# Kernel optimization log

Hardware: AMD Instinct MI355X
Metric: run time of the kernel (lower is better)

The kernel has to match this reference:

```python
import jax, jax.numpy as jnp
import numpy as np

C = 5.0          # tanh clamp constant (args.c, non-trainable)
B, N, R, D = 4, 16, 64, 256  # batch, block_num, block_len, word_dim
NEG = -1e9


def setup_inputs() -> dict:
    key = jax.random.key(0)
    ks = iter(jax.random.split(key, 80))

    def W(i, o):
        # xavier-like init (torch stores (out,in); we store (in,out) and use x @ W)
        return jax.random.normal(next(ks), (i, o), jnp.float32) * np.float32(np.sqrt(2.0 / (i + o)))

    def bvec(d):
        return jax.random.normal(next(ks), (d,), jnp.float32) * 0.01

    inp = {"x": jax.random.normal(next(ks), (B, N, R, D), jnp.float32)}
    for p in ("fw", "bw"):
        inp[f"fcW_{p}"] = W(D, D);  inp[f"fcb_{p}"] = bvec(D)
        inp[f"mW1_{p}"] = W(D, D);  inp[f"mW2_{p}"] = W(D, D);  inp[f"mb_{p}"] = bvec(D)
        inp[f"s2tW1_{p}"] = W(D, D); inp[f"s2tb1_{p}"] = bvec(D)
        inp[f"s2tW_{p}"] = W(D, D);  inp[f"s2tb_{p}"] = bvec(D)
        inp[f"gW1_{p}"] = W(D, D);  inp[f"gW2_{p}"] = W(D, D);  inp[f"gb_{p}"] = bvec(D)
        inp[f"fW1_{p}"] = W(3 * D, D); inp[f"fb1_{p}"] = bvec(D)
        inp[f"fW2_{p}"] = W(3 * D, D); inp[f"fb2_{p}"] = bvec(D)
    return inp


def _mSA(x, W1, W2, b, fw):
    # x: (..., L, d) -> (..., L, d). Additive per-feature attention with strict
    # triangular mask. fw: token i attends to j > i (last row zeroed);
    # bw: token i attends to j < i (first row zeroed). Matches the torch
    # -inf mask + narrow + zero-pad construction exactly.
    L = x.shape[-2]
    xi = (x @ W1)[..., :, None, :]                 # (..., L, 1, d)
    xj = (x @ W2)[..., None, :, :]                 # (..., 1, L, d)
    f = C * jnp.tanh((xi + xj + b) / C)            # (..., i, j, d)
    i = jnp.arange(L)[:, None]
    j = jnp.arange(L)[None, :]
    allowed = (j > i) if fw else (j < i)           # (L, L)
    scores = jnp.where(allowed[..., None], f, NEG)
    att = jax.nn.softmax(scores, axis=-2)          # softmax over j
    rowvalid = (jnp.arange(L) < L - 1) if fw else (jnp.arange(L) > 0)
    att = att * rowvalid[:, None, None].astype(x.dtype)
    return jnp.einsum('...ijd,...jd->...id', att, x)


def _s2t(x, W1, b1, Wo, bo):
    # source2token self-attention: (..., L, d) -> (..., d)
    f = jax.nn.relu(x @ W1 + b1)
    a = jax.nn.softmax(f @ Wo + bo, axis=-2)
    return jnp.sum(a * x, axis=-2)


def _mblosa(x, mW1, mW2, mb, s2tW1, s2tb1, s2tW, s2tb,
            gW1, gW2, gb, fW1, fb1, fW2, fb2, fw):
    Bb, n, r, d = x.shape
    h = _mSA(x, mW1, mW2, mb, fw)                  # (B, n, r, d) intra-block
    v = _s2t(h, s2tW1, s2tb1, s2tW, s2tb)          # (B, n, d)    block summary
    o = _mSA(v, mW1, mW2, mb, fw)                  # (B, n, d)    inter-block
    G = jax.nn.sigmoid(o @ gW1 + v @ gW2 + gb)
    e = G * o + (1.0 - G) * v                      # (B, n, d)
    # torch: cat of e[i] repeated r times, then narrow(1, 0, n)
    idx = jnp.arange(n) // r
    E = e[:, idx]                                  # (B, n, d)
    # torch: flatten blocks then narrow(1, 0, n) (faithful to source)
    xf = x.reshape(Bb, n * r, d)[:, :n]
    hf = h.reshape(Bb, n * r, d)[:, :n]
    cat = jnp.concatenate([xf, hf, E], axis=-1)    # (B, n, 3d)
    fusion = jax.nn.relu(cat @ fW1 + fb1)
    Gf = jax.nn.sigmoid(cat @ fW2 + fb2)
    return Gf * fusion + (1.0 - Gf) * xf           # (B, n, d)


def reference(x,
              fcW_fw, fcb_fw, mW1_fw, mW2_fw, mb_fw, s2tW1_fw, s2tb1_fw,
              s2tW_fw, s2tb_fw, gW1_fw, gW2_fw, gb_fw, fW1_fw, fb1_fw,
              fW2_fw, fb2_fw,
              fcW_bw, fcb_bw, mW1_bw, mW2_bw, mb_bw, s2tW1_bw, s2tb1_bw,
              s2tW_bw, s2tb_bw, gW1_bw, gW2_bw, gb_bw, fW1_bw, fb1_bw,
              fW2_bw, fb2_bw):
    in_fw = jax.nn.relu(x @ fcW_fw + fcb_fw)
    in_bw = jax.nn.relu(x @ fcW_bw + fcb_bw)
    u_fw = _mblosa(in_fw, mW1_fw, mW2_fw, mb_fw, s2tW1_fw, s2tb1_fw,
                   s2tW_fw, s2tb_fw, gW1_fw, gW2_fw, gb_fw,
                   fW1_fw, fb1_fw, fW2_fw, fb2_fw, True)
    u_bw = _mblosa(in_bw, mW1_bw, mW2_bw, mb_bw, s2tW1_bw, s2tb1_bw,
                   s2tW_bw, s2tb_bw, gW1_bw, gW2_bw, gb_bw,
                   fW1_bw, fb1_bw, fW2_bw, fb2_bw, False)
    return jnp.concatenate([u_fw, u_bw], axis=-1)  # (B, n, 2d)
```

## Files before the change

### kernel.cpp

```cpp
#include <hip/hip_runtime.h>
#include <hip/hip_bf16.h>

typedef __hip_bfloat16 BF16;
typedef __attribute__((ext_vector_type(8))) short short8;
typedef __attribute__((ext_vector_type(4))) float f32x4;

#define MFMA_B16(a,b,c) __builtin_amdgcn_mfma_f32_16x16x32_bf16((a),(b),(c),0,0,0)

#if __has_builtin(__builtin_amdgcn_exp2f)
#define EXP2F(x) __builtin_amdgcn_exp2f(x)
#else
#define EXP2F(x) __expf(0.6931471805599453f * (x))
#endif

__device__ __forceinline__ short f2bs(float f){ BF16 h = __float2bfloat16(f); return *(short*)&h; }
__device__ __forceinline__ float bs2f(short s){ BF16 h = *(BF16*)&s; return __bfloat162float(h); }

struct SrcPack { const float* s[10]; };

__global__ __launch_bounds__(256) void prep_k(SrcPack p, short* __restrict__ Oh,
                                              short* __restrict__ Ol)
{
    __shared__ float s[64][65];
    const float* W = p.s[blockIdx.y];
    short* oh = Oh + (size_t)blockIdx.y * 65536;
    short* ol = Ol + (size_t)blockIdx.y * 65536;
    int tr = (blockIdx.x >> 2) * 64, tc = (blockIdx.x & 3) * 64;
    #pragma unroll
    for (int i = 0; i < 16; i++) {
        int e = threadIdx.x + i * 256;
        int r = e >> 6, c = e & 63;
        s[c][r] = W[(size_t)(tr + r) * 256 + tc + c];
    }
    __syncthreads();
    #pragma unroll
    for (int i = 0; i < 16; i++) {
        int e = threadIdx.x + i * 256;
        int c2 = e >> 6, r2 = e & 63;
        float v = s[c2][r2];
        short hi = f2bs(v);
        short lo = f2bs(v - bs2f(hi));
        size_t oi = (size_t)(tc + c2) * 256 + tr + r2;
        oh[oi] = hi;
        ol[oi] = lo;
    }
}

template<int AM, int OM, int RELU, int BS>
__device__ __forceinline__ void gemm_body(const void* __restrict__ A0,
    const void* __restrict__ Alo,
    const short* __restrict__ Wh, const short* __restrict__ Wl,
    const float* __restrict__ bias, void* __restrict__ O0, void* __restrict__ O1,
    int row0, int col0)
{
    constexpr int LDK = 72;
    __shared__ short sAh[64 * LDK];
    __shared__ short sAl[(AM == 0) ? 8 : 64 * LDK];
    __shared__ short sBh[64 * LDK];
    __shared__ short sBl[BS ? 8 : 64 * LDK];
    int tid = threadIdx.x;
    int w = tid >> 6, l = tid & 63;
    int m = l & 15, q = l >> 4;
    int sr = w * 16 + m;

    f32x4 acc[4];
    #pragma unroll
    for (int cf = 0; cf < 4; cf++) acc[cf] = (f32x4)(0.f);

    for (int kh = 0; kh < 4; kh++) {
        int kbase = kh * 64;
        #pragma unroll
        for (int i = 0; i < 2; i++) {
            int kl = q * 8 + 32 * i;
            size_t gofs = (size_t)(row0 + sr) * 256 + kbase + kl;
            if (AM == 1) {
                const float* src = (const float*)A0 + gofs;
                float4 f0 = *(const float4*)src;
                float4 f1 = *(const float4*)(src + 4);
                short8 vh, vl;
                float tmp[8] = {f0.x, f0.y, f0.z, f0.w, f1.x, f1.y, f1.z, f1.w};
                #pragma unroll
                for (int j = 0; j < 8; j++) {
                    vh[j] = f2bs(tmp[j]);
                    vl[j] = f2bs(tmp[j] - bs2f(vh[j]));
                }
                *(short8*)&sAh[sr * LDK + kl] = vh;
                *(short8*)&sAl[sr * LDK + kl] = vl;
            } else if (AM == 2) {
                *(short8*)&sAh[sr * LDK + kl] = *(const short8*)((const short*)A0 + gofs);
                *(short8*)&sAl[sr * LDK + kl] = *(const short8*)((const short*)Alo + gofs);
            } else {
                *(short8*)&sAh[sr * LDK + kl] = *(const short8*)((const short*)A0 + gofs);
            }
            size_t gofsB = (size_t)(col0 + sr) * 256 + kbase + kl;
            *(short8*)&sBh[sr * LDK + kl] = *(const short8*)(Wh + gofsB);
            if (!BS)
                *(short8*)&sBl[sr * LDK + kl] = *(const short8*)(Wl + gofsB);
        }
        __syncthreads();
        #pragma unroll
        for (int ch = 0; ch < 2; ch++) {
            int k = ch * 32 + q * 8;
            short8 ah = *(const short8*)&sAh[(w * 16 + m) * LDK + k];
            short8 al = (AM != 0) ? *(const short8*)&sAl[(w * 16 + m) * LDK + k] : ah;
            #pragma unroll
            for (int cf = 0; cf < 4; cf++) {
                short8 bh = *(const short8*)&sBh[(cf * 16 + m) * LDK + k];
                acc[cf] = MFMA_B16(ah, bh, acc[cf]);
                if (!BS) {
                    short8 bl = *(const short8*)&sBl[(cf * 16 + m) * LDK + k];
                    acc[cf] = MFMA_B16(ah, bl, acc[cf]);
                }
                if (AM != 0)
                    acc[cf] = MFMA_B16(al, bh, acc[cf]);
            }
        }
        __syncthreads();
    }
    #pragma unroll
    for (int cf = 0; cf < 4; cf++) {
        int col = col0 + cf * 16 + m;
        float bv = bias ? bias[col] : 0.f;
        #pragma unroll
        for (int r = 0; r < 4; r++) {
            int row = row0 + w * 16 + q * 4 + r;
            float v = acc[cf][r] + bv;
            if (RELU) v = fmaxf(v, 0.f);
            size_t oi = (size_t)row * 256 + col;
            if (OM == 0) {
                ((float*)O0)[oi] = v;
            } else if (OM == 1) {
                ((short*)O0)[oi] = f2bs(v);
            } else {
                short hi = f2bs(v);
                ((short*)O0)[oi] = hi;
                ((short*)O1)[oi] = f2bs(v - bs2f(hi));
            }
        }
    }
}

struct GDir { const void* A0; const void* Al; const short* Wh; const short* Wl;
              const float* bias; void* O0; void* O1; };

template<int AM, int OM, int RELU, int BS>
__global__ __launch_bounds__(256) void gemm_k(GDir p0, GDir p1)
{
    GDir p = blockIdx.z ? p1 : p0;
    gemm_body<AM, OM, RELU, BS>(p.A0, p.Al, p.Wh, p.Wl, p.bias, p.O0, p.O1,
                                blockIdx.x * 64, blockIdx.y * 64);
}

struct MbloDir { const short* Ah;
                 const short* W1h; const short* W2h;
                 const float* mb; short* Hh; int fw; };

__global__ __launch_bounds__(512) void mblo_k(MbloDir p0, MbloDir p1)
{
    __shared__ char smraw[33536] __attribute__((aligned(16)));
    short* gAh  = (short*)smraw;
    short* gB1h = gAh + 4608;
    short* gB2h = gAh + 9216;
    float* aP   = (float*)smraw;
    unsigned int* aQX = (unsigned int*)(smraw + 16896);

    const float KLN = -0.06931471805599453f;

    MbloDir p = blockIdx.z ? p1 : p0;
    int tid = threadIdx.x;
    int w = tid >> 6, l = tid & 63;
    int m = l & 15, q = l >> 4;
    int rh = w >> 1;
    int cb = (w & 1) * 2;
    int bn = blockIdx.x >> 1, ipar = blockIdx.x & 1;
    int row0 = bn * 64, d0 = blockIdx.y * 64;
    int srow = tid >> 3;
    int skl  = (tid & 7) * 8;

    f32x4 acc1[2], acc2[2];
    #pragma unroll
    for (int cf = 0; cf < 2; cf++) { acc1[cf] = (f32x4)(0.f); acc2[cf] = (f32x4)(0.f); }

    for (int kh = 0; kh < 4; kh++) {
        int kbase = kh * 64;
        size_t ga = (size_t)(row0 + srow) * 256 + kbase + skl;
        *(short8*)&gAh[srow * 72 + skl] = *(const short8*)(p.Ah + ga);
        size_t gb = (size_t)(d0 + srow) * 256 + kbase + skl;
        *(short8*)&gB1h[srow * 72 + skl] = *(const short8*)(p.W1h + gb);
        *(short8*)&gB2h[srow * 72 + skl] = *(const short8*)(p.W2h + gb);
        __syncthreads();
        #pragma unroll
        for (int ch = 0; ch < 2; ch++) {
            int k = ch * 32 + q * 8;
            short8 ah = *(const short8*)&gAh[(rh * 16 + m) * 72 + k];
            #pragma unroll
            for (int cf = 0; cf < 2; cf++) {
                int bofs = ((cb + cf) * 16 + m) * 72 + k;
                short8 b1 = *(const short8*)&gB1h[bofs];
                acc1[cf] = MFMA_B16(ah, b1, acc1[cf]);
                short8 b2 = *(const short8*)&gB2h[bofs];
                acc2[cf] = MFMA_B16(ah, b2, acc2[cf]);
            }
        }
        __syncthreads();
    }
    short* sQX = (short*)aQX;
    #pragma unroll
    for (int cf = 0; cf < 2; cf++) {
        int col = (cb + cf) * 16 + m;
        float mbv = p.mb[d0 + col];
        #pragma unroll
        for (int r = 0; r < 4; r++) {
            int row = rh * 16 + q * 4 + r;
            aP[row * 66 + col] = __expf(0.4f * acc1[cf][r]) * KLN;
            sQX[col * 130 + 2 * row] = f2bs(__expf(0.4f * (acc2[cf][r] + mbv)));
        }
    }
    {
        size_t gx = (size_t)(row0 + srow) * 256 + d0 + skl;
        short8 xh = *(const short8*)(p.Ah + gx);
        #pragma unroll
        for (int t = 0; t < 8; t++)
            sQX[(skl + t) * 130 + 2 * srow + 1] = xh[t];
    }
    __syncthreads();
    const unsigned int* lane_qx = &aQX[l * 65];
    #pragma unroll
    for (int t8 = 0; t8 < 4; t8++) {
        int i = ipar + 2 * (w + 8 * t8);
        float Pp = aP[i * 66 + l];
        int js = p.fw ? (i + 1) : 0;
        int je = p.fw ? 64 : i;
        float den0 = 0.f, den1 = 0.f, num0 = 0.f, num1 = 0.f;
        int j = js;
        for (; j + 4 <= je; j += 4) {
            unsigned int u0 = lane_qx[j];
            unsigned int u1 = lane_qx[j + 1];
            unsigned int u2 = lane_qx[j + 2];
            unsigned int u3 = lane_qx[j + 3];
            float q0 = bs2f((short)(u0 & 0xffff)), x0 = bs2f((short)(u0 >> 16));
            float q1 = bs2f((short)(u1 & 0xffff)), x1 = bs2f((short)(u1 >> 16));
            float q2 = bs2f((short)(u2 & 0xffff)), x2 = bs2f((short)(u2 >> 16));
            float q3 = bs2f((short)(u3 & 0xffff)), x3 = bs2f((short)(u3 >> 16));
            float w0 = EXP2F(__builtin_amdgcn_rcpf(fmaf(Pp, q0, KLN)));
            float w1 = EXP2F(__builtin_amdgcn_rcpf(fmaf(Pp, q1, KLN)));
            float w2 = EXP2F(__builtin_amdgcn_rcpf(fmaf(Pp, q2, KLN)));
            float w3 = EXP2F(__builtin_amdgcn_rcpf(fmaf(Pp, q3, KLN)));
            den0 += w0; num0 = fmaf(w0, x0, num0);
            den1 += w1; num1 = fmaf(w1, x1, num1);
            den0 += w2; num0 = fmaf(w2, x2, num0);
            den1 += w3; num1 = fmaf(w3, x3, num1);
        }
        for (; j < je; j++) {
            unsigned int u0 = lane_qx[j];
            float q0 = bs2f((short)(u0 & 0xffff)), x0 = bs2f((short)(u0 >> 16));
            float wgt = EXP2F(__builtin_amdgcn_rcpf(fmaf(Pp, q0, KLN)));
            den0 += wgt; num0 = fmaf(wgt, x0, num0);
        }
        float den = den0 + den1, num = num0 + num1;
        bool valid = p.fw ? (i < 63) : (i > 0);
        float out = valid ? (num * __builtin_amdgcn_rcpf(den)) : 0.f;
        p.Hh[(size_t)(row0 + i) * 256 + d0 + l] = f2bs(out);
    }
}

struct S2TDir { const short* Hh; const short* W3h; const float* b1;
                const short* W4h; const float* b2; float* V; };

__global__ __launch_bounds__(512) void s2t_fused_k(S2TDir p0, S2TDir p1)
{
    __shared__ char smraw[79872] __attribute__((aligned(16)));
    short* sT1 = (short*)smraw;
    short* gA  = (short*)(smraw + 33792);
    short* gB  = (short*)(smraw + 43008);
    short* gB2 = (short*)(smraw + 33792);
    float* aL  = (float*)(smraw + 43008);
    float* rm  = (float*)(smraw + 60416);
    float* rd  = rm + 512;
    float* rn  = rm + 1024;

    S2TDir p = blockIdx.z ? p1 : p0;
    int tid = threadIdx.x;
    int w = tid >> 6, l = tid & 63;
    int m = l & 15, q = l >> 4;
    int row0 = blockIdx.x * 64;
    int strip = w >> 1, chalf = w & 1;
    int srow = tid >> 3, skl = (tid & 7) * 8;

    f32x4 acc1[8];
    #pragma unroll
    for (int cf = 0; cf < 8; cf++) acc1[cf] = (f32x4)(0.f);
    for (int kh = 0; kh < 4; kh++) {
        int kbase = kh * 64;
        *(short8*)&gA[srow * 72 + skl] =
            *(const short8*)(p.Hh + (size_t)(row0 + srow) * 256 + kbase + skl);
        int bn = tid >> 1;
        #pragma unroll
        for (int i = 0; i < 4; i++) {
            int kseg = (tid & 1) * 32 + i * 8;
            *(short8*)&gB[bn * 72 + kseg] =
                *(const short8*)(p.W3h + (size_t)bn * 256 + kbase + kseg);
        }
        __syncthreads();
        #pragma unroll
        for (int ch = 0; ch < 2; ch++) {
            int k = ch * 32 + q * 8;
            short8 ah = *(const short8*)&gA[(strip * 16 + m) * 72 + k];
            #pragma unroll
            for (int cf = 0; cf < 8; cf++) {
                short8 bh = *(const short8*)&gB[(chalf * 128 + cf * 16 + m) * 72 + k];
                acc1[cf] = MFMA_B16(ah, bh, acc1[cf]);
            }
        }
        __syncthreads();
    }
    #pragma unroll
    for (int cf = 0; cf < 8; cf++) {
        int col = chalf * 128 + cf * 16 + m;
        float bv = p.b1[col];
        #pragma unroll
        for (int r = 0; r < 4; r++) {
            int row = strip * 16 + q * 4 + r;
            sT1[row * 264 + col] = f2bs(fmaxf(acc1[cf][r] + bv, 0.f));
        }
    }
    __syncthreads();

    for (int dc = 0; dc < 2; dc++) {
        int d0 = (blockIdx.y * 2 + dc) * 64;
        f32x4 acc2[2];
        acc2[0] = (f32x4)(0.f); acc2[1] = (f32x4)(0.f);
        for (int kh = 0; kh < 4; kh++) {
            int kbase = kh * 64;
            *(short8*)&gB2[srow * 72 + skl] =
                *(const short8*)(p.W4h + (size_t)(d0 + srow) * 256 + kbase + skl);
            __syncthreads();
            #pragma unroll
            for (int ch = 0; ch < 2; ch++) {
                int k = ch * 32 + q * 8;
                short8 ah = *(const short8*)&sT1[(strip * 16 + m) * 264 + kbase + k];
                #pragma unroll
                for (int cf = 0; cf < 2; cf++) {
                    short8 bh = *(const short8*)&gB2[(chalf * 32 + cf * 16 + m) * 72 + k];
                    acc2[cf] = MFMA_B16(ah, bh, acc2[cf]);
                }
            }
            __syncthreads();
        }
        #pragma unroll
        for (int cf = 0; cf < 2; cf++) {
            int col = chalf * 32 + cf * 16 + m;
            float bv = p.b2[d0 + col];
            #pragma unroll
            for (int r = 0; r < 4; r++) {
                int row = strip * 16 + q * 4 + r;
                aL[row * 68 + col] = acc2[cf][r] + bv;
            }
        }
        __syncthreads();
        int dl = tid & 63, rq = tid >> 6;
        float mx = -1e30f, den = 0.f, num = 0.f;
        #pragma unroll
        for (int rr = 0; rr < 8; rr++) {
            int r = rq * 8 + rr;
            float lv = aL[r * 68 + dl];
            float hv = bs2f(p.Hh[(size_t)(row0 + r) * 256 + d0 + dl]);
            if (lv > mx) { float sc = __expf(mx - lv); den *= sc; num *= sc; mx = lv; }
            float wgt = __expf(lv - mx);
            den += wgt; num = fmaf(wgt, hv, num);
        }
        rm[rq * 64 + dl] = mx; rd[rq * 64 + dl] = den; rn[rq * 64 + dl] = num;
        __syncthreads();
        if (rq == 0) {
            float M = rm[dl];
            #pragma unroll
            for (int kq = 1; kq < 8; kq++) M = fmaxf(M, rm[kq * 64 + dl]);
            float D = 0.f, Nn = 0.f;
            #pragma unroll
            for (int kq = 0; kq < 8; kq++) {
                float sc = __expf(rm[kq * 64 + dl] - M);
                D += rd[kq * 64 + dl] * sc;
                Nn += rn[kq * 64 + dl] * sc;
            }
            p.V[(size_t)blockIdx.x * 256 + d0 + dl] = Nn / D;
        }
        __syncthreads();
    }
}

struct Gate2Dir { const float* V; const float* W1; const float* W2; const float* mb;
                  const float* gW1; const float* gW2; const float* gb;
                  float* E0; int fw; };

__global__ __launch_bounds__(512) void attn2gate_k(Gate2Dir p0, Gate2Dir p1)
{
    Gate2Dir p = blockIdx.z ? p1 : p0;
    __shared__ __attribute__((aligned(16))) float sVT[4096];
    __shared__ float sPart[16][256];
    __shared__ float so[256], sv[256], red[8][64];
    int tid = threadIdx.x;
    int b = blockIdx.x;
    int k = tid & 255, half = tid >> 8;

    if (p.fw) {
        #pragma unroll
        for (int it = 0; it < 8; it++) {
            int e = tid + it * 512;
            int kk = e >> 4, j = e & 15;
            sVT[e] = p.V[(size_t)(b * 16 + j) * 256 + kk];
        }
        __syncthreads();
        float acc[16];
        #pragma unroll
        for (int j = 0; j < 16; j++) acc[j] = 0.f;
        int kk0 = half * 128;
        #pragma unroll 4
        for (int kk = kk0; kk < kk0 + 128; kk++) {
            const float4* vr = (const float4*)&sVT[kk * 16];
            float4 va = vr[0], vb = vr[1], vc = vr[2], vd = vr[3];
            float w1 = p.W1[(size_t)kk * 256 + k];
            float w2 = p.W2[(size_t)kk * 256 + k];
            acc[0]  = fmaf(va.x, w1, acc[0]);
            acc[1]  = fmaf(va.y, w2, acc[1]);
            acc[2]  = fmaf(va.z, w2, acc[2]);
            acc[3]  = fmaf(va.w, w2, acc[3]);
            acc[4]  = fmaf(vb.x, w2, acc[4]);
            acc[5]  = fmaf(vb.y, w2, acc[5]);
            acc[6]  = fmaf(vb.z, w2, acc[6]);
            acc[7]  = fmaf(vb.w, w2, acc[7]);
            acc[8]  = fmaf(vc.x, w2, acc[8]);
            acc[9]  = fmaf(vc.y, w2, acc[9]);
            acc[10] = fmaf(vc.z, w2, acc[10]);
            acc[11] = fmaf(vc.w, w2, acc[11]);
            acc[12] = fmaf(vd.x, w2, acc[12]);
            acc[13] = fmaf(vd.y, w2, acc[13]);
            acc[14] = fmaf(vd.z, w2, acc[14]);
            acc[15] = fmaf(vd.w, w2, acc[15]);
        }
        if (half) {
            #pragma unroll
            for (int j = 0; j < 16; j++) sPart[j][k] = acc[j];
        }
        __syncthreads();
        if (!half) {
            #pragma unroll
            for (int j = 0; j < 16; j++) acc[j] += sPart[j][k];
            float base = acc[0] + p.mb[k];
            float den = 0.f, num = 0.f;
            #pragma unroll
            for (int j = 1; j < 16; j++) {
                float z = (base + acc[j]) * 0.2f;
                float e2 = __expf(2.f * z);
                float t = 1.f - 2.f / (e2 + 1.f);
                float wgt = __expf(5.f * t);
                den += wgt;
                num = fmaf(wgt, p.V[(size_t)(b * 16 + j) * 256 + k], num);
            }
            so[k] = num / den;
            sv[k] = p.V[(size_t)(b * 16) * 256 + k];
        }
    } else {
        if (!half) {
            so[k] = 0.f;
            sv[k] = p.V[(size_t)(b * 16) * 256 + k];
        }
    }
    __syncthreads();
    int c = tid & 63, ks = tid >> 6;
    int gc = blockIdx.y * 64 + c;
    float a2 = 0.f;
    int k0 = ks * 32;
    #pragma unroll 8
    for (int kkx = 0; kkx < 32; kkx++) {
        int kx = k0 + kkx;
        a2 += so[kx] * p.gW1[(size_t)kx * 256 + gc] + sv[kx] * p.gW2[(size_t)kx * 256 + gc];
    }
    red[ks][c] = a2;
    __syncthreads();
    if (ks == 0) {
        float a = red[0][c] + red[1][c] + red[2][c] + red[3][c]
                + red[4][c] + red[5][c] + red[6][c] + red[7][c] + p.gb[gc];
        float G = 1.f / (1.f + __expf(-a));
        p.E0[b * 256 + gc] = G * so[gc] + (1.f - G) * sv[gc];
    }
}

struct FuseDir { const short* INh; const short* Hh;
                 const float* E0; const float* fW1; const float* fb1;
                 const float* fW2; const float* fb2; };

__global__ __launch_bounds__(256) void fusion_k(FuseDir p0, FuseDir p1, float* __restrict__ out)
{
    FuseDir p = blockIdx.z ? p1 : p0;
    __shared__ float cat[768];
    __shared__ float red1[4][64], red2[4][64];
    int bt = blockIdx.x, b = bt >> 4, t = bt & 15;
    int c = threadIdx.x & 63, ks = threadIdx.x >> 6;
    int gc = blockIdx.y * 64 + c;
    size_t xrow = ((size_t)b * 1024 + t) * 256;
    cat[threadIdx.x]       = bs2f(p.INh[xrow + threadIdx.x]);
    cat[256 + threadIdx.x] = bs2f(p.Hh[xrow + threadIdx.x]);
    cat[512 + threadIdx.x] = p.E0[b * 256 + threadIdx.x];
    __syncthreads();
    float a1 = 0.f, a2 = 0.f;
    int k0 = ks * 192;
    #pragma unroll 8
    for (int kk = 0; kk < 192; kk++) {
        int k = k0 + kk;
        float cv = cat[k];
        a1 += cv * p.fW1[(size_t)k * 256 + gc];
        a2 += cv * p.fW2[(size_t)k * 256 + gc];
    }
    red1[ks][c] = a1; red2[ks][c] = a2;
    __syncthreads();
    if (ks == 0) {
        float s1 = red1[0][c] + red1[1][c] + red1[2][c] + red1[3][c] + p.fb1[gc];
        float s2 = red2[0][c] + red2[1][c] + red2[2][c] + red2[3][c] + p.fb2[gc];
        float fus = fmaxf(s1, 0.f);
        float Gf = 1.f / (1.f + __expf(-s2));
        float u = Gf * fus + (1.f - Gf) * cat[gc];
        out[((size_t)(b * 16 + t)) * 512 + (size_t)blockIdx.z * 256 + gc] = u;
    }
}

extern "C" void kernel_launch(void* const* d_in, const int* in_sizes, int n_in,
                              void* d_out, int out_size, void* d_ws, size_t ws_size,
                              hipStream_t stream)
{
    const float* x = (const float*)d_in[0];
    char* base = (char*)d_ws;
    auto alloc = [&](size_t bytes){ void* r = base; base += (bytes + 255) & ~255ULL; return r; };
    short* inH = (short*)alloc(2 * 1048576 * 2);
    short* hH  = (short*)alloc(2 * 1048576 * 2);
    short* wtH = (short*)alloc(10 * 65536 * 2);
    short* wtL = (short*)alloc(10 * 65536 * 2);
    float* v   = (float*)alloc(2 * 16384 * 4);
    float* E0  = (float*)alloc(2 * 1024 * 4);

    SrcPack sp;
    const int src_idx[5] = {0, 2, 3, 5, 7};
    for (int p = 0; p < 2; p++)
        for (int i = 0; i < 5; i++)
            sp.s[p * 5 + i] = (const float*)d_in[1 + p * 16 + src_idx[i]];
    prep_k<<<dim3(16, 10), 256, 0, stream>>>(sp, wtH, wtL);

    GDir fc[2];
    MbloDir mbd[2];
    S2TDir std[2];
    Gate2Dir gtd[2];
    FuseDir fsd[2];
    for (int p = 0; p < 2; p++) {
        int bi = 1 + p * 16;
        const float* fcb   = (const float*)d_in[bi + 1];
        const float* mb    = (const float*)d_in[bi + 4];
        const float* s2tb1 = (const float*)d_in[bi + 6];
        const float* s2tb  = (const float*)d_in[bi + 8];
        size_t po = (size_t)p * 1048576;
        const short* W0h = wtH + (size_t)(p * 5 + 0) * 65536, *W0l = wtL + (size_t)(p * 5 + 0) * 65536;
        const short* W1h = wtH + (size_t)(p * 5 + 1) * 65536;
        const short* W2h = wtH + (size_t)(p * 5 + 2) * 65536;
        const short* W3h = wtH + (size_t)(p * 5 + 3) * 65536;
        const short* W4h = wtH + (size_t)(p * 5 + 4) * 65536;

        fc[p]   = { x, nullptr, W0h, W0l, fcb, inH + po, nullptr };
        mbd[p]  = { inH + po, W1h, W2h, mb, hH + po, (p == 0) };
        std[p]  = { hH + po, W3h, s2tb1, W4h, s2tb, v + p * 16384 };
        gtd[p]  = { v + p * 16384,
                    (const float*)d_in[bi + 2], (const float*)d_in[bi + 3], mb,
                    (const float*)d_in[bi + 9], (const float*)d_in[bi + 10],
                    (const float*)d_in[bi + 11], E0 + p * 1024, (p == 0) };
        fsd[p]  = { inH + po, hH + po, E0 + p * 1024,
                    (const float*)d_in[bi + 12], (const float*)d_in[bi + 13],
                    (const float*)d_in[bi + 14], (const float*)d_in[bi + 15] };
    }

    gemm_k<1, 1, 1, 0><<<dim3(64, 4, 2), 256, 0, stream>>>(fc[0], fc[1]);
    mblo_k<<<dim3(128, 4, 2), 512, 0, stream>>>(mbd[0], mbd[1]);
    s2t_fused_k<<<dim3(64, 2, 2), 512, 0, stream>>>(std[0], std[1]);
    attn2gate_k<<<dim3(4, 4, 2), 512, 0, stream>>>(gtd[0], gtd[1]);
    fusion_k<<<dim3(64, 4, 2), 256, 0, stream>>>(fsd[0], fsd[1], (float*)d_out);
}
```

Before: 207.8 us.

## Pre-split x to bf16 hi/lo once and rebalance work splits across kernels

The fp32 x is split into bf16 hi/lo pairs once in the prep kernel, so the fc GEMM blocks for each direction stop redoing that conversion. mblo_k no longer splits rows by parity across two blocks; each block now handles all 64 query rows, which halves its grid. s2t_fused_k moves its per-block dc loop into the grid by doubling grid.y, and attn2gate_k goes to 1024 threads with a four-way k split. These trade redundant conversion and A/B-operand reloads for more parallelism, at the cost of extra workspace traffic and different occupancy per kernel.

```diff
diff --git a/kernel.cpp b/kernel.cpp
--- a/kernel.cpp
+++ b/kernel.cpp
@@ -3,6 +3,7 @@
 
 typedef __hip_bfloat16 BF16;
 typedef __attribute__((ext_vector_type(8))) short short8;
+typedef __attribute__((ext_vector_type(4))) short short4v;
 typedef __attribute__((ext_vector_type(4))) float f32x4;
 
 #define MFMA_B16(a,b,c) __builtin_amdgcn_mfma_f32_16x16x32_bf16((a),(b),(c),0,0,0)
@@ -18,9 +19,31 @@
 
 struct SrcPack { const float* s[10]; };
 
-__global__ __launch_bounds__(256) void prep_k(SrcPack p, short* __restrict__ Oh,
-                                              short* __restrict__ Ol)
-{
+__global__ __launch_bounds__(256) void prep_k(SrcPack p, const float* __restrict__ X,
+                                              short* __restrict__ Oh,
+                                              short* __restrict__ Ol,
+                                              short* __restrict__ Xh,
+                                              short* __restrict__ Xl)
+{
+    if (blockIdx.y >= 10) {
+        int u = (blockIdx.y - 10) * 16 + blockIdx.x;
+        size_t base = (size_t)u * 16384;
+        #pragma unroll
+        for (int i = 0; i < 16; i++) {
+            size_t idx = base + (size_t)i * 1024 + threadIdx.x * 4;
+            float4 f = *(const float4*)(X + idx);
+            short4v vh, vl;
+            float t0[4] = {f.x, f.y, f.z, f.w};
+            #pragma unroll
+            for (int j = 0; j < 4; j++) {
+                vh[j] = f2bs(t0[j]);
+                vl[j] = f2bs(t0[j] - bs2f(vh[j]));
+            }
+            *(short4v*)(Xh + idx) = vh;
+            *(short4v*)(Xl + idx) = vl;
+        }
+        return;
+    }
     __shared__ float s[64][65];
     const float* W = p.s[blockIdx.y];
     short* oh = Oh + (size_t)blockIdx.y * 65536;
@@ -50,7 +73,7 @@
 __device__ __forceinline__ void gemm_body(const void* __restrict__ A0,
     const void* __restrict__ Alo,
     const short* __restrict__ Wh, const short* __restrict__ Wl,
-    const float* __restrict__ bias, void* __restrict__ O0, void* __restrict__ O1,
+    const float* __restrict__ bias, void* __restrict__ O0,
     int row0, int col0)
 {
     constexpr int LDK = 72;
@@ -73,20 +96,7 @@
         for (int i = 0; i < 2; i++) {
             int kl = q * 8 + 32 * i;
             size_t gofs = (size_t)(row0 + sr) * 256 + kbase + kl;
-            if (AM == 1) {
-                const float* src = (const float*)A0 + gofs;
-                float4 f0 = *(const float4*)src;
-                float4 f1 = *(const float4*)(src + 4);
-                short8 vh, vl;
-                float tmp[8] = {f0.x, f0.y, f0.z, f0.w, f1.x, f1.y, f1.z, f1.w};
-                #pragma unroll
-                for (int j = 0; j < 8; j++) {
-                    vh[j] = f2bs(tmp[j]);
-                    vl[j] = f2bs(tmp[j] - bs2f(vh[j]));
-                }
-                *(short8*)&sAh[sr * LDK + kl] = vh;
-                *(short8*)&sAl[sr * LDK + kl] = vl;
-            } else if (AM == 2) {
+            if (AM == 2) {
                 *(short8*)&sAh[sr * LDK + kl] = *(const short8*)((const short*)A0 + gofs);
                 *(short8*)&sAl[sr * LDK + kl] = *(const short8*)((const short*)Alo + gofs);
             } else {
@@ -129,25 +139,21 @@
             size_t oi = (size_t)row * 256 + col;
             if (OM == 0) {
                 ((float*)O0)[oi] = v;
-            } else if (OM == 1) {
+            } else {
                 ((short*)O0)[oi] = f2bs(v);
-            } else {
-                short hi = f2bs(v);
-                ((short*)O0)[oi] = hi;
-                ((short*)O1)[oi] = f2bs(v - bs2f(hi));
             }
         }
     }
 }
 
 struct GDir { const void* A0; const void* Al; const short* Wh; const short* Wl;
-              const float* bias; void* O0; void* O1; };
+              const float* bias; void* O0; };
 
 template<int AM, int OM, int RELU, int BS>
 __global__ __launch_bounds__(256) void gemm_k(GDir p0, GDir p1)
 {
     GDir p = blockIdx.z ? p1 : p0;
-    gemm_body<AM, OM, RELU, BS>(p.A0, p.Al, p.Wh, p.Wl, p.bias, p.O0, p.O1,
+    gemm_body<AM, OM, RELU, BS>(p.A0, p.Al, p.Wh, p.Wl, p.bias, p.O0,
                                 blockIdx.x * 64, blockIdx.y * 64);
 }
 
@@ -172,8 +178,7 @@
     int m = l & 15, q = l >> 4;
     int rh = w >> 1;
     int cb = (w & 1) * 2;
-    int bn = blockIdx.x >> 1, ipar = blockIdx.x & 1;
-    int row0 = bn * 64, d0 = blockIdx.y * 64;
+    int row0 = blockIdx.x * 64, d0 = blockIdx.y * 64;
     int srow = tid >> 3;
     int skl  = (tid & 7) * 8;
 
@@ -225,9 +230,8 @@
     }
     __syncthreads();
     const unsigned int* lane_qx = &aQX[l * 65];
-    #pragma unroll
-    for (int t8 = 0; t8 < 4; t8++) {
-        int i = ipar + 2 * (w + 8 * t8);
+    for (int t8 = 0; t8 < 8; t8++) {
+        int i = w + 8 * t8;
         float Pp = aP[i * 66 + l];
         int js = p.fw ? (i + 1) : 0;
         int je = p.fw ? 64 : i;
@@ -284,6 +288,7 @@
     int w = tid >> 6, l = tid & 63;
     int m = l & 15, q = l >> 4;
     int row0 = blockIdx.x * 64;
+    int d0 = blockIdx.y * 64;
     int strip = w >> 1, chalf = w & 1;
     int srow = tid >> 3, skl = (tid & 7) * 8;
 
@@ -326,65 +331,61 @@
     }
     __syncthreads();
 
-    for (int dc = 0; dc < 2; dc++) {
-        int d0 = (blockIdx.y * 2 + dc) * 64;
-        f32x4 acc2[2];
-        acc2[0] = (f32x4)(0.f); acc2[1] = (f32x4)(0.f);
-        for (int kh = 0; kh < 4; kh++) {
-            int kbase = kh * 64;
-            *(short8*)&gB2[srow * 72 + skl] =
-                *(const short8*)(p.W4h + (size_t)(d0 + srow) * 256 + kbase + skl);
-            __syncthreads();
-            #pragma unroll
-            for (int ch = 0; ch < 2; ch++) {
-                int k = ch * 32 + q * 8;
-                short8 ah = *(const short8*)&sT1[(strip * 16 + m) * 264 + kbase + k];
-                #pragma unroll
-                for (int cf = 0; cf < 2; cf++) {
-                    short8 bh = *(const short8*)&gB2[(chalf * 32 + cf * 16 + m) * 72 + k];
-                    acc2[cf] = MFMA_B16(ah, bh, acc2[cf]);
-                }
-            }
-            __syncthreads();
-        }
-        #pragma unroll
-        for (int cf = 0; cf < 2; cf++) {
-            int col = chalf * 32 + cf * 16 + m;
-            float bv = p.b2[d0 + col];
-            #pragma unroll
-            for (int r = 0; r < 4; r++) {
-                int row = strip * 16 + q * 4 + r;
-                aL[row * 68 + col] = acc2[cf][r] + bv;
-            }
-        }
-        __syncthreads();
-        int dl = tid & 63, rq = tid >> 6;
-        float mx = -1e30f, den = 0.f, num = 0.f;
-        #pragma unroll
-        for (int rr = 0; rr < 8; rr++) {
-            int r = rq * 8 + rr;
-            float lv = aL[r * 68 + dl];
-            float hv = bs2f(p.Hh[(size_t)(row0 + r) * 256 + d0 + dl]);
-            if (lv > mx) { float sc = __expf(mx - lv); den *= sc; num *= sc; mx = lv; }
-            float wgt = __expf(lv - mx);
-            den += wgt; num = fmaf(wgt, hv, num);
-        }
-        rm[rq * 64 + dl] = mx; rd[rq * 64 + dl] = den; rn[rq * 64 + dl] = num;
-        __syncthreads();
-        if (rq == 0) {
-            float M = rm[dl];
-            #pragma unroll
-            for (int kq = 1; kq < 8; kq++) M = fmaxf(M, rm[kq * 64 + dl]);
-            float D = 0.f, Nn = 0.f;
-            #pragma unroll
-            for (int kq = 0; kq < 8; kq++) {
-                float sc = __expf(rm[kq * 64 + dl] - M);
-                D += rd[kq * 64 + dl] * sc;
-                Nn += rn[kq * 64 + dl] * sc;
-            }
-            p.V[(size_t)blockIdx.x * 256 + d0 + dl] = Nn / D;
-        }
-        __syncthreads();
+    f32x4 acc2[2];
+    acc2[0] = (f32x4)(0.f); acc2[1] = (f32x4)(0.f);
+    for (int kh = 0; kh < 4; kh++) {
+        int kbase = kh * 64;
+        *(short8*)&gB2[srow * 72 + skl] =
+            *(const short8*)(p.W4h + (size_t)(d0 + srow) * 256 + kbase + skl);
+        __syncthreads();
+        #pragma unroll
+        for (int ch = 0; ch < 2; ch++) {
+            int k = ch * 32 + q * 8;
+            short8 ah = *(const short8*)&sT1[(strip * 16 + m) * 264 + kbase + k];
+            #pragma unroll
+            for (int cf = 0; cf < 2; cf++) {
+                short8 bh = *(const short8*)&gB2[(chalf * 32 + cf * 16 + m) * 72 + k];
+                acc2[cf] = MFMA_B16(ah, bh, acc2[cf]);
+            }
+        }
+        __syncthreads();
+    }
+    #pragma unroll
+    for (int cf = 0; cf < 2; cf++) {
+        int col = chalf * 32 + cf * 16 + m;
+        float bv = p.b2[d0 + col];
+        #pragma unroll
+        for (int r = 0; r < 4; r++) {
+            int row = strip * 16 + q * 4 + r;
+            aL[row * 68 + col] = acc2[cf][r] + bv;
+        }
+    }
+    __syncthreads();
+    int dl = tid & 63, rq = tid >> 6;
+    float mx = -1e30f, den = 0.f, num = 0.f;
+    #pragma unroll
+    for (int rr = 0; rr < 8; rr++) {
+        int r = rq * 8 + rr;
+        float lv = aL[r * 68 + dl];
+        float hv = bs2f(p.Hh[(size_t)(row0 + r) * 256 + d0 + dl]);
+        if (lv > mx) { float sc = __expf(mx - lv); den *= sc; num *= sc; mx = lv; }
+        float wgt = __expf(lv - mx);
+        den += wgt; num = fmaf(wgt, hv, num);
+    }
+    rm[rq * 64 + dl] = mx; rd[rq * 64 + dl] = den; rn[rq * 64 + dl] = num;
+    __syncthreads();
+    if (rq == 0) {
+        float M = rm[dl];
+        #pragma unroll
+        for (int kq = 1; kq < 8; kq++) M = fmaxf(M, rm[kq * 64 + dl]);
+        float D = 0.f, Nn = 0.f;
+        #pragma unroll
+        for (int kq = 0; kq < 8; kq++) {
+            float sc = __expf(rm[kq * 64 + dl] - M);
+            D += rd[kq * 64 + dl] * sc;
+            Nn += rn[kq * 64 + dl] * sc;
+        }
+        p.V[(size_t)blockIdx.x * 256 + d0 + dl] = Nn / D;
     }
 }
 
@@ -392,20 +393,20 @@
                   const float* gW1; const float* gW2; const float* gb;
                   float* E0; int fw; };
 
-__global__ __launch_bounds__(512) void attn2gate_k(Gate2Dir p0, Gate2Dir p1)
+__global__ __launch_bounds__(1024) void attn2gate_k(Gate2Dir p0, Gate2Dir p1)
 {
     Gate2Dir p = blockIdx.z ? p1 : p0;
     __shared__ __attribute__((aligned(16))) float sVT[4096];
-    __shared__ float sPart[16][256];
-    __shared__ float so[256], sv[256], red[8][64];
+    __shared__ float sPart[3][16][256];
+    __shared__ float so[256], sv[256], red[16][64];
     int tid = threadIdx.x;
     int b = blockIdx.x;
-    int k = tid & 255, half = tid >> 8;
+    int k = tid & 255, quarter = tid >> 8;
 
     if (p.fw) {
         #pragma unroll
-        for (int it = 0; it < 8; it++) {
-            int e = tid + it * 512;
+        for (int it = 0; it < 4; it++) {
+            int e = tid + it * 1024;
             int kk = e >> 4, j = e & 15;
             sVT[e] = p.V[(size_t)(b * 16 + j) * 256 + kk];
         }
@@ -413,9 +414,9 @@
         float acc[16];
         #pragma unroll
         for (int j = 0; j < 16; j++) acc[j] = 0.f;
-        int kk0 = half * 128;
+        int kk0 = quarter * 64;
         #pragma unroll 4
-        for (int kk = kk0; kk < kk0 + 128; kk++) {
+        for (int kk = kk0; kk < kk0 + 64; kk++) {
             const float4* vr = (const float4*)&sVT[kk * 16];
             float4 va = vr[0], vb = vr[1], vc = vr[2], vd = vr[3];
             float w1 = p.W1[(size_t)kk * 256 + k];
@@ -437,14 +438,15 @@
             acc[14] = fmaf(vd.z, w2, acc[14]);
             acc[15] = fmaf(vd.w, w2, acc[15]);
         }
-        if (half) {
-            #pragma unroll
-            for (int j = 0; j < 16; j++) sPart[j][k] = acc[j];
-        }
-        __syncthreads();
-        if (!half) {
-            #pragma unroll
-            for (int j = 0; j < 16; j++) acc[j] += sPart[j][k];
+        if (quarter) {
+            #pragma unroll
+            for (int j = 0; j < 16; j++) sPart[quarter - 1][j][k] = acc[j];
+        }
+        __syncthreads();
+        if (!quarter) {
+            #pragma unroll
+            for (int j = 0; j < 16; j++)
+                acc[j] += sPart[0][j][k] + sPart[1][j][k] + sPart[2][j][k];
             float base = acc[0] + p.mb[k];
             float den = 0.f, num = 0.f;
             #pragma unroll
@@ -460,7 +462,7 @@
             sv[k] = p.V[(size_t)(b * 16) * 256 + k];
         }
     } else {
-        if (!half) {
+        if (tid < 256) {
             so[k] = 0.f;
             sv[k] = p.V[(size_t)(b * 16) * 256 + k];
         }
@@ -469,17 +471,18 @@
     int c = tid & 63, ks = tid >> 6;
     int gc = blockIdx.y * 64 + c;
     float a2 = 0.f;
-    int k0 = ks * 32;
-    #pragma unroll 8
-    for (int kkx = 0; kkx < 32; kkx++) {
+    int k0 = ks * 16;
+    #pragma unroll
+    for (int kkx = 0; kkx < 16; kkx++) {
         int kx = k0 + kkx;
         a2 += so[kx] * p.gW1[(size_t)kx * 256 + gc] + sv[kx] * p.gW2[(size_t)kx * 256 + gc];
     }
     red[ks][c] = a2;
     __syncthreads();
     if (ks == 0) {
-        float a = red[0][c] + red[1][c] + red[2][c] + red[3][c]
-                + red[4][c] + red[5][c] + red[6][c] + red[7][c] + p.gb[gc];
+        float a = p.gb[gc];
+        #pragma unroll
+        for (int kq = 0; kq < 16; kq++) a += red[kq][c];
         float G = 1.f / (1.f + __expf(-a));
         p.E0[b * 256 + gc] = G * so[gc] + (1.f - G) * sv[gc];
     }
@@ -534,6 +537,8 @@
     short* hH  = (short*)alloc(2 * 1048576 * 2);
     short* wtH = (short*)alloc(10 * 65536 * 2);
     short* wtL = (short*)alloc(10 * 65536 * 2);
+    short* xh  = (short*)alloc(1048576 * 2);
+    short* xl  = (short*)alloc(1048576 * 2);
     float* v   = (float*)alloc(2 * 16384 * 4);
     float* E0  = (float*)alloc(2 * 1024 * 4);
 
@@ -542,11 +547,11 @@
     for (int p = 0; p < 2; p++)
         for (int i = 0; i < 5; i++)
             sp.s[p * 5 + i] = (const float*)d_in[1 + p * 16 + src_idx[i]];
-    prep_k<<<dim3(16, 10), 256, 0, stream>>>(sp, wtH, wtL);
+    prep_k<<<dim3(16, 14), 256, 0, stream>>>(sp, x, wtH, wtL, xh, xl);
 
     GDir fc[2];
     MbloDir mbd[2];
-    S2TDir std[2];
+    S2TDir std_[2];
     Gate2Dir gtd[2];
     FuseDir fsd[2];
     for (int p = 0; p < 2; p++) {
@@ -562,9 +567,9 @@
         const short* W3h = wtH + (size_t)(p * 5 + 3) * 65536;
         const short* W4h = wtH + (size_t)(p * 5 + 4) * 65536;
 
-        fc[p]   = { x, nullptr, W0h, W0l, fcb, inH + po, nullptr };
+        fc[p]   = { xh, xl, W0h, W0l, fcb, inH + po };
         mbd[p]  = { inH + po, W1h, W2h, mb, hH + po, (p == 0) };
-        std[p]  = { hH + po, W3h, s2tb1, W4h, s2tb, v + p * 16384 };
+        std_[p] = { hH + po, W3h, s2tb1, W4h, s2tb, v + p * 16384 };
         gtd[p]  = { v + p * 16384,
                     (const float*)d_in[bi + 2], (const float*)d_in[bi + 3], mb,
                     (const float*)d_in[bi + 9], (const float*)d_in[bi + 10],
@@ -574,9 +579,9 @@
                     (const float*)d_in[bi + 14], (const float*)d_in[bi + 15] };
     }
 
-    gemm_k<1, 1, 1, 0><<<dim3(64, 4, 2), 256, 0, stream>>>(fc[0], fc[1]);
-    mblo_k<<<dim3(128, 4, 2), 512, 0, stream>>>(mbd[0], mbd[1]);
-    s2t_fused_k<<<dim3(64, 2, 2), 512, 0, stream>>>(std[0], std[1]);
-    attn2gate_k<<<dim3(4, 4, 2), 512, 0, stream>>>(gtd[0], gtd[1]);
+    gemm_k<2, 1, 1, 0><<<dim3(64, 4, 2), 256, 0, stream>>>(fc[0], fc[1]);
+    mblo_k<<<dim3(64, 4, 2), 512, 0, stream>>>(mbd[0], mbd[1]);
+    s2t_fused_k<<<dim3(64, 4, 2), 512, 0, stream>>>(std_[0], std_[1]);
+    attn2gate_k<<<dim3(4, 4, 2), 1024, 0, stream>>>(gtd[0], gtd[1]);
     fusion_k<<<dim3(64, 4, 2), 256, 0, stream>>>(fsd[0], fsd[1], (float*)d_out);
 }
```

Result: slower. 220.4 us (+6.0%).
